# Optimization experiments

Hardware: AMD Instinct MI355X
Metric: run time of the kernel (lower is better)

The kernel has to match this reference:

```python
import jax, jax.numpy as jnp
import numpy as np


def _direction(x, W_in, conv_w, conv_b, W_xproj, A_log, D, W_out):
    # x: [b, l, d_model]
    b, L, _ = x.shape
    d_inner = A_log.shape[0]
    xz = x @ W_in.T                         # [b, l, 2*d_inner]
    xc, z = jnp.split(xz, 2, axis=-1)
    # depthwise causal conv1d (left pad d_conv-1, keep first L outputs)
    xt = jnp.transpose(xc, (0, 2, 1))       # [b, d_inner, l]
    k = conv_w.shape[-1]
    xt = jax.lax.conv_general_dilated(
        xt, conv_w, window_strides=(1,), padding=[(k - 1, 0)],
        dimension_numbers=("NCH", "OIH", "NCH"), feature_group_count=d_inner)
    xt = xt + conv_b[None, :, None]
    xc = jax.nn.silu(jnp.transpose(xt, (0, 2, 1)))  # [b, l, d_inner]
    proj = xc @ W_xproj.T                   # [b, l, d_inner + 2*n]
    n = (proj.shape[-1] - d_inner) // 2
    delta = jax.nn.softplus(proj[..., :d_inner])
    Bm = proj[..., d_inner:d_inner + n]
    Cm = proj[..., d_inner + n:]
    A = -jnp.exp(A_log)                     # [d_inner]

    def step(s, inp):
        u_t, dt, B_t, C_t = inp             # [b,d], [b,d], [b,n], [b,n]
        dA = jnp.exp(dt[..., None] * A[None, :, None])          # [b,d,n]
        s = dA * s + dt[..., None] * B_t[:, None, :] * u_t[..., None]
        y = jnp.einsum('bn,bdn->bd', C_t, s) + D * u_t
        return s, y

    s0 = jnp.zeros((b, d_inner, n), x.dtype)
    xs = (jnp.swapaxes(xc, 0, 1), jnp.swapaxes(delta, 0, 1),
          jnp.swapaxes(Bm, 0, 1), jnp.swapaxes(Cm, 0, 1))
    _, ys = jax.lax.scan(step, s0, xs)      # ys: [l, b, d_inner]
    y = jnp.swapaxes(ys, 0, 1)
    y = y * jax.nn.silu(z)
    return y @ W_out.T                      # [b, l, d_model]


def setup_inputs() -> dict:
    key = jax.random.key(0)
    ks = jax.random.split(key, 8)
    b, L, d_model, d_inner, n, k = 2, 1024, 512, 1024, 64, 4
    s = lambda kk, shape, sc=0.02: jax.random.normal(kk, shape, jnp.float32) * sc
    return {
        "x": jax.random.normal(ks[0], (b, L, d_model), jnp.float32),
        "W_in": s(ks[1], (2 * d_inner, d_model)),
        "conv_w": s(ks[2], (d_inner, 1, k), 0.1),
        "conv_b": s(ks[3], (d_inner,), 0.1),
        "W_xproj": s(ks[4], (d_inner + 2 * n, d_inner)),
        "A_log": jax.random.normal(ks[5], (d_inner,), jnp.float32),
        "D": jnp.ones((d_inner,), jnp.float32),
        "W_out": s(ks[6], (d_model, d_inner)),
    }


def reference(x, W_in, conv_w, conv_b, W_xproj, A_log, D, W_out):
    out_fwd = _direction(x, W_in, conv_w, conv_b, W_xproj, A_log, D, W_out)
    out_bwd = _direction(jnp.flip(x, axis=1), W_in, conv_w, conv_b, W_xproj, A_log, D, W_out)
    return 0.5 * (out_fwd + jnp.flip(out_bwd, axis=1))
```

## Files before the change

### kernel.cpp

```cpp
#include <hip/hip_runtime.h>
#include <math.h>

#define B_    2
#define LSEQ  1024
#define DM    512
#define DI    1024
#define NS    64
#define TC    32
#define NC    (LSEQ/TC)
#define LDP   72

typedef __bf16 bf16x8 __attribute__((ext_vector_type(8)));
typedef float  f32x4  __attribute__((ext_vector_type(4)));

__device__ __forceinline__ float fexp(float x)   { return __expf(x); }
__device__ __forceinline__ float sp_f(float x)   { return fmaxf(x, 0.f) + __logf(1.f + __expf(-fabsf(x))); }
__device__ __forceinline__ float silu_f(float x) { return x * __builtin_amdgcn_rcpf(1.f + __expf(-x)); }
__device__ __forceinline__ unsigned short f2bf(float f) {
    unsigned int u = __float_as_uint(f);
    u += 0x7FFF + ((u >> 16) & 1);
    return (unsigned short)(u >> 16);
}
__device__ __forceinline__ float bf2f(unsigned short h) {
    return __uint_as_float(((unsigned int)h) << 16);
}
__device__ __forceinline__ void gload16(const void* g, void* l) {
    __builtin_amdgcn_global_load_lds(
        (const __attribute__((address_space(1))) unsigned int*)g,
        (__attribute__((address_space(3))) unsigned int*)l, 16, 0, 0);
}

__global__ __launch_bounds__(256) void castall(
    const float* __restrict__ x, const float* __restrict__ W_in,
    const float* __restrict__ W_xproj, const float* __restrict__ W_out,
    unsigned short* __restrict__ xb, unsigned short* __restrict__ winb,
    unsigned short* __restrict__ wxb, unsigned short* __restrict__ wob)
{
    int i = (blockIdx.x * 256 + threadIdx.x) * 4;
    const float* s; unsigned short* dst; int off;
    if (i < 1048576)      { s = x;       dst = xb;   off = i; }
    else if (i < 2097152) { s = W_in;    dst = winb; off = i - 1048576; }
    else if (i < 3276800) { s = W_xproj; dst = wxb;  off = i - 2097152; }
    else                  { s = W_out;   dst = wob;  off = i - 3276800; }
    float4 v = *(const float4*)(s + off);
    ushort4 o;
    o.x = f2bf(v.x); o.y = f2bf(v.y); o.z = f2bf(v.z); o.w = f2bf(v.w);
    *(ushort4*)(dst + off) = o;
}

__global__ __launch_bounds__(256) void gemm64(
    const unsigned short* __restrict__ Alo, const unsigned short* __restrict__ Ahi,
    const unsigned short* __restrict__ B, float* __restrict__ C,
    int M, int N, int K, int wrapK, int ks, int mode,
    const float* __restrict__ A_log, const unsigned short* __restrict__ u_in,
    unsigned* __restrict__ ddu_out,
    unsigned short* __restrict__ Bbf, unsigned short* __restrict__ Cbf)
{
    __shared__ short As0[64 * 64];
    __shared__ short Bs0[64 * 64];
    __shared__ short As1[64 * 64];
    __shared__ short Bs1[64 * 64];
    const int tid  = threadIdx.x;
    const int lane = tid & 63, wid = tid >> 6;

    const int gx = gridDim.x;
    int id  = blockIdx.y * gx + blockIdx.x;
    int q   = (gx * gridDim.y) >> 3;
    int swz = (id & 7) * q + (id >> 3);
    const int bm = (swz / gx) * 64, bn = (swz % gx) * 64;

    const int wm = (wid >> 1) * 32, wn = (wid & 1) * 32;
    const int fr = lane & 15;
    const int h  = fr & 7;
    const int tq = lane >> 4;
    const int Kc = K / ks;
    const int k0beg = blockIdx.z * Kc;
    const int nsteps = Kc / 64;
    float* Cz = C + (size_t)blockIdx.z * M * N;
    unsigned short* Czb = (unsigned short*)C + (size_t)blockIdx.z * M * N;

    const unsigned short* Asrc;
    int ka0;
    if (k0beg >= wrapK) { Asrc = Ahi; ka0 = k0beg - wrapK; }
    else                { Asrc = Alo; ka0 = k0beg; }

    const char* pA[2];
    const char* pB[2];
#pragma unroll
    for (int r = 0; r < 2; r++) {
        int o    = tid * 16 + r * 4096;
        int row  = o >> 7;
        int colb = ((((o >> 4) & 7) ^ (row & 7)) << 4);
        pA[r] = (const char*)Asrc + ((size_t)(bm + row) * wrapK + ka0) * 2 + colb;
        pB[r] = (const char*)B    + ((size_t)(bn + row) * wrapK + ka0) * 2 + colb;
    }
    const int wbase = wid * 1024;

    f32x4 acc[2][2];
#pragma unroll
    for (int i = 0; i < 2; i++)
#pragma unroll
        for (int j = 0; j < 2; j++) acc[i][j] = (f32x4)0.f;

    auto STAGE = [&](short* Adst, short* Bdst) {
#pragma unroll
        for (int r = 0; r < 2; r++) { gload16(pA[r], (char*)Adst + wbase + r * 4096); pA[r] += 128; }
#pragma unroll
        for (int r = 0; r < 2; r++) { gload16(pB[r], (char*)Bdst + wbase + r * 4096); pB[r] += 128; }
    };
    auto COMPUTE = [&](const short* Asrc_l, const short* Bsrc_l) {
#pragma unroll
        for (int kk = 0; kk < 2; kk++) {
            const int sc = ((kk * 4 + tq) ^ h) << 3;
            bf16x8 af[2], bfr[2];
#pragma unroll
            for (int i = 0; i < 2; i++)
                af[i] = *reinterpret_cast<const bf16x8*>(&Asrc_l[(wm + i * 16 + fr) * 64 + sc]);
#pragma unroll
            for (int j = 0; j < 2; j++)
                bfr[j] = *reinterpret_cast<const bf16x8*>(&Bsrc_l[(wn + j * 16 + fr) * 64 + sc]);
#pragma unroll
            for (int i = 0; i < 2; i++)
#pragma unroll
                for (int j = 0; j < 2; j++)
                    acc[i][j] = __builtin_amdgcn_mfma_f32_16x16x32_bf16(af[i], bfr[j], acc[i][j], 0, 0, 0);
        }
    };

    STAGE(As0, Bs0);
    __syncthreads();
    for (int st = 0; st < nsteps; st += 2) {
        if (st + 1 < nsteps) STAGE(As1, Bs1);
        COMPUTE(As0, Bs0);
        __syncthreads();
        if (st + 1 < nsteps) {
            if (st + 2 < nsteps) STAGE(As0, Bs0);
            COMPUTE(As1, Bs1);
            __syncthreads();
        }
    }

    const int crow = (lane >> 4) * 4;
    if (mode == 2) {
        if (bn < 1024) {
#pragma unroll
            for (int j = 0; j < 2; j++) {
                int d = bn + wn + j * 16 + fr;
                float nAd = -fexp(A_log[d]);
#pragma unroll
                for (int i = 0; i < 2; i++)
#pragma unroll
                    for (int r = 0; r < 4; r++) {
                        int m = bm + wm + i * 16 + crow + r;
                        float delta = sp_f(acc[i][j][r]);
                        size_t idx = (size_t)m * DI + d;
                        float dA = fexp(delta * nAd);
                        float du = delta * bf2f(u_in[idx]);
                        ddu_out[idx] = (unsigned)f2bf(dA) | ((unsigned)f2bf(du) << 16);
                    }
            }
        } else {
#pragma unroll
            for (int j = 0; j < 2; j++) {
                int cc = bn + wn + j * 16 + fr;
#pragma unroll
                for (int i = 0; i < 2; i++)
#pragma unroll
                    for (int r = 0; r < 4; r++) {
                        int m = bm + wm + i * 16 + crow + r;
                        unsigned short v16 = f2bf(acc[i][j][r]);
                        if (cc < 1024 + NS) Bbf[(size_t)m * NS + cc - 1024]      = v16;
                        else                Cbf[(size_t)m * NS + cc - 1024 - NS] = v16;
                    }
            }
        }
    } else {
#pragma unroll
        for (int i = 0; i < 2; i++)
#pragma unroll
            for (int j = 0; j < 2; j++)
#pragma unroll
                for (int r = 0; r < 4; r++) {
                    size_t idx = (size_t)(bm + wm + i * 16 + crow + r) * N + (bn + wn + j * 16 + fr);
                    if (mode == 1) Czb[idx] = f2bf(acc[i][j][r]);
                    else           Cz[idx]  = acc[i][j][r];
                }
    }
}

__global__ __launch_bounds__(256) void reduce4(
    const float* __restrict__ p, float* __restrict__ out, int n)
{
    int i = (blockIdx.x * 256 + threadIdx.x) * 4;
    if (i >= n) return;
    float4 a = *(const float4*)(p + i);
    float4 b = *(const float4*)(p + n + i);
    float4 c = *(const float4*)(p + 2 * n + i);
    float4 d = *(const float4*)(p + 3 * n + i);
    float4 o;
    o.x = (a.x + b.x) + (c.x + d.x);
    o.y = (a.y + b.y) + (c.y + d.y);
    o.z = (a.z + b.z) + (c.z + d.z);
    o.w = (a.w + b.w) + (c.w + d.w);
    *(float4*)(out + i) = o;
}

__global__ __launch_bounds__(256) void convk(
    const unsigned short* __restrict__ xzb, const float* __restrict__ cw,
    const float* __restrict__ cb, const float* __restrict__ Dvec,
    unsigned short* __restrict__ uc2b, unsigned short* __restrict__ ygb,
    unsigned short* __restrict__ Fbuf)
{
    int idx = blockIdx.x * 256 + threadIdx.x;
    int b   = idx >> 18;
    int rem = idx & ((LSEQ * 256) - 1);
    int tau = rem >> 8;
    int d4  = (rem & 255) << 2;

    const unsigned short* xc = xzb + (size_t)b * LSEQ * (2 * DI);
    float xv[7][4];
#pragma unroll
    for (int rr = 0; rr < 7; rr++) {
        int t = tau - 3 + rr;
        if (t >= 0 && t < LSEQ) {
            ushort4 v = *(const ushort4*)&xc[(size_t)t * 2048 + d4];
            xv[rr][0] = bf2f(v.x); xv[rr][1] = bf2f(v.y);
            xv[rr][2] = bf2f(v.z); xv[rr][3] = bf2f(v.w);
        } else {
            xv[rr][0] = 0.f; xv[rr][1] = 0.f; xv[rr][2] = 0.f; xv[rr][3] = 0.f;
        }
    }
    ushort4 zv = *(const ushort4*)&xc[(size_t)tau * 2048 + DI + d4];
    float4 cbv = *(const float4*)&cb[d4];
    float4 Dv  = *(const float4*)&Dvec[d4];
    float cbA[4] = {cbv.x, cbv.y, cbv.z, cbv.w};
    float DA[4]  = {Dv.x, Dv.y, Dv.z, Dv.w};
    float zA[4]  = {bf2f(zv.x), bf2f(zv.y), bf2f(zv.z), bf2f(zv.w)};

    unsigned short ufb[4], ubb[4], yfb[4], ybb[4], Ff[4];
#pragma unroll
    for (int j = 0; j < 4; j++) {
        float4 w = *(const float4*)&cw[(size_t)(d4 + j) * 4];
        float accf = fmaf(w.x, xv[0][j], fmaf(w.y, xv[1][j], fmaf(w.z, xv[2][j], fmaf(w.w, xv[3][j], cbA[j]))));
        float accb = fmaf(w.x, xv[6][j], fmaf(w.y, xv[5][j], fmaf(w.z, xv[4][j], fmaf(w.w, xv[3][j], cbA[j]))));
        float uf = silu_f(accf), ub = silu_f(accb);
        ufb[j] = f2bf(uf); ubb[j] = f2bf(ub);
        yfb[j] = f2bf(DA[j] * uf); ybb[j] = f2bf(DA[j] * ub);
        Ff[j]  = f2bf(0.5f * silu_f(zA[j]));
    }
    size_t fi = ((size_t)b * LSEQ + tau) * DI + d4;
    size_t bi = ((size_t)(2 + b) * LSEQ + tau) * DI + d4;
    *(ushort4*)&uc2b[fi] = *(ushort4*)ufb;
    *(ushort4*)&uc2b[bi] = *(ushort4*)ubb;
    *(ushort4*)&ygb[fi]  = *(ushort4*)yfb;
    *(ushort4*)&ygb[bi]  = *(ushort4*)ybb;
    *(ushort4*)&Fbuf[fi] = *(ushort4*)Ff;
}

__global__ __launch_bounds__(256) void passA(
    const unsigned* __restrict__ ddu,
    const unsigned short* __restrict__ Bbf, const unsigned short* __restrict__ Cbf,
    unsigned short* __restrict__ ygb, unsigned short* __restrict__ gbuf,
    unsigned short* __restrict__ sEnd, float* __restrict__ Pbuf)
{
    const int dl   = threadIdx.x >> 2;
    const int nq   = threadIdx.x & 3;
    const int d0   = blockIdx.x * 64;
    const int d    = d0 + dl;
    const int c    = blockIdx.y;
    const int dirb = blockIdx.z;
    const int dir  = dirb >> 1;

    __shared__ float Bsh[TC][NS];
    __shared__ float Csh[TC][NS];
    __shared__ unsigned short gshY[TC][64];
    __shared__ unsigned short gshG[TC][64];

    for (int i = threadIdx.x * 4; i < TC * NS; i += 1024) {
        int tl = i >> 6, n = i & 63;
        int tau = dir ? (LSEQ - 1 - (c * TC + tl)) : (c * TC + tl);
        ushort4 vb = *(const ushort4*)&Bbf[((size_t)dirb * LSEQ + tau) * NS + n];
        ushort4 vc = *(const ushort4*)&Cbf[((size_t)dirb * LSEQ + tau) * NS + n];
        Bsh[tl][n+0] = bf2f(vb.x); Bsh[tl][n+1] = bf2f(vb.y);
        Bsh[tl][n+2] = bf2f(vb.z); Bsh[tl][n+3] = bf2f(vb.w);
        Csh[tl][n+0] = bf2f(vc.x); Csh[tl][n+1] = bf2f(vc.y);
        Csh[tl][n+2] = bf2f(vc.z); Csh[tl][n+3] = bf2f(vc.w);
    }
    __syncthreads();

    float s[16];
#pragma unroll
    for (int i = 0; i < 16; i++) s[i] = 0.f;
    float g_run = 1.f;

    int tau0 = dir ? (LSEQ - 1 - c * TC) : (c * TC);
    long stp = (dir ? -1L : 1L) * (long)DI;
    const unsigned* pW = ddu + ((size_t)dirb * LSEQ + tau0) * DI + d;
    const unsigned short* pY = ygb + ((size_t)dirb * LSEQ + tau0) * DI + d;

    unsigned w = *pW;
    float Du = bf2f(*pY);
    for (int tl = 0; tl < TC; tl++) {
        unsigned w_c = w;
        float Du_c = Du;
        if (tl + 1 < TC) {
            pW += stp; pY += stp;
            w = *pW; Du = bf2f(*pY);
        }
        float dA_c = bf2f((unsigned short)(w_c & 0xffff));
        float du_c = bf2f((unsigned short)(w_c >> 16));
        g_run *= dA_c;
        float ydot = 0.f;
        const float4* brow = (const float4*)&Bsh[tl][nq * 16];
        const float4* crow = (const float4*)&Csh[tl][nq * 16];
#pragma unroll
        for (int q = 0; q < 4; q++) {
            float4 bv = brow[q];
            float4 cv = crow[q];
            float s0 = fmaf(du_c, bv.x, dA_c * s[4*q+0]); s[4*q+0] = s0; ydot = fmaf(cv.x, s0, ydot);
            float s1 = fmaf(du_c, bv.y, dA_c * s[4*q+1]); s[4*q+1] = s1; ydot = fmaf(cv.y, s1, ydot);
            float s2 = fmaf(du_c, bv.z, dA_c * s[4*q+2]); s[4*q+2] = s2; ydot = fmaf(cv.z, s2, ydot);
            float s3 = fmaf(du_c, bv.w, dA_c * s[4*q+3]); s[4*q+3] = s3; ydot = fmaf(cv.w, s3, ydot);
        }
        ydot += __shfl_xor(ydot, 1);
        ydot += __shfl_xor(ydot, 2);
        if (nq == 0) {
            gshY[tl][dl] = f2bf(Du_c + ydot);
            gshG[tl][dl] = f2bf(g_run);
        }
    }
    __syncthreads();

    size_t base = (((size_t)dirb * NC + c) * DI + d) * NS + nq * 16;
#pragma unroll
    for (int q = 0; q < 4; q++) {
        ushort4 v;
        v.x = f2bf(s[4*q+0]); v.y = f2bf(s[4*q+1]);
        v.z = f2bf(s[4*q+2]); v.w = f2bf(s[4*q+3]);
        *(ushort4*)&sEnd[base + q * 4] = v;
    }
    if (nq == 0) Pbuf[((size_t)dirb * NC + c) * DI + d] = g_run;

    for (int i = threadIdx.x * 4; i < TC * 64; i += 1024) {
        int tl = i >> 6, col = i & 63;
        int tau = dir ? (LSEQ - 1 - (c * TC + tl)) : (c * TC + tl);
        *(ushort4*)&ygb[((size_t)dirb * LSEQ + tau) * DI + d0 + col]  = *(const ushort4*)&gshY[tl][col];
        *(ushort4*)&gbuf[((size_t)dirb * LSEQ + tau) * DI + d0 + col] = *(const ushort4*)&gshG[tl][col];
    }
}

__global__ __launch_bounds__(256) void passB(
    const unsigned* __restrict__ sEnd2, const float* __restrict__ Pbuf,
    unsigned* __restrict__ sInit2)
{
    const int fl   = blockIdx.x * 256 + threadIdx.x;
    const int dirb = blockIdx.y;
    const int d    = fl >> 5;
    float r0 = 0.f, r1 = 0.f;
    for (int c = 0; c < NC; c++) {
        size_t idx = ((size_t)(dirb * NC + c)) * (DI * NS / 2) + fl;
        unsigned v = sEnd2[idx];
        float t0 = bf2f((unsigned short)(v & 0xffff));
        float t1 = bf2f((unsigned short)(v >> 16));
        sInit2[idx] = (unsigned)f2bf(r0) | ((unsigned)f2bf(r1) << 16);
        float P = Pbuf[((size_t)dirb * NC + c) * DI + d];
        r0 = fmaf(P, r0, t0);
        r1 = fmaf(P, r1, t1);
    }
}

__global__ __launch_bounds__(256) void corrK(
    const unsigned short* __restrict__ Cbf, const unsigned short* __restrict__ sInitB,
    const unsigned short* __restrict__ gbuf, const unsigned short* __restrict__ Fbuf,
    unsigned short* __restrict__ ygb)
{
    const int tid  = threadIdx.x;
    const int lane = tid & 63, wid = tid >> 6;
    const int d0   = blockIdx.x * 128;
    const int c    = blockIdx.y;
    const int dirb = blockIdx.z;
    const int dir  = dirb >> 1;
    const int b    = dirb & 1;
    const int fr = lane & 15, fk = (lane >> 4) * 8;
    const int wn = wid * 32;

    __shared__ short Cs[TC * LDP];
    __shared__ short Ss[128 * LDP];
    __shared__ float corrS[TC * 128];

    for (int i = tid * 4; i < TC * 64; i += 1024) {
        int tl = i >> 6, n = i & 63;
        int tau = dir ? (LSEQ - 1 - (c * TC + tl)) : (c * TC + tl);
        *(ushort4*)&Cs[tl * LDP + n] = *(const ushort4*)&Cbf[((size_t)dirb * LSEQ + tau) * NS + n];
    }
    for (int i = tid * 4; i < 128 * 64; i += 1024) {
        int r = i >> 6, n = i & 63;
        *(ushort4*)&Ss[r * LDP + n] =
            *(const ushort4*)&sInitB[(((size_t)dirb * NC + c) * DI + d0 + r) * NS + n];
    }
    __syncthreads();

    f32x4 acc[2][2];
#pragma unroll
    for (int i = 0; i < 2; i++)
#pragma unroll
        for (int j = 0; j < 2; j++) acc[i][j] = (f32x4)0.f;

#pragma unroll
    for (int kk = 0; kk < 2; kk++) {
        bf16x8 af[2], bfr[2];
#pragma unroll
        for (int i = 0; i < 2; i++)
            af[i] = *reinterpret_cast<const bf16x8*>(&Cs[(i * 16 + fr) * LDP + kk * 32 + fk]);
#pragma unroll
        for (int j = 0; j < 2; j++)
            bfr[j] = *reinterpret_cast<const bf16x8*>(&Ss[(wn + j * 16 + fr) * LDP + kk * 32 + fk]);
#pragma unroll
        for (int i = 0; i < 2; i++)
#pragma unroll
            for (int j = 0; j < 2; j++)
                acc[i][j] = __builtin_amdgcn_mfma_f32_16x16x32_bf16(af[i], bfr[j], acc[i][j], 0, 0, 0);
    }

    const int crow = (lane >> 4) * 4;
#pragma unroll
    for (int i = 0; i < 2; i++)
#pragma unroll
        for (int j = 0; j < 2; j++)
#pragma unroll
            for (int r = 0; r < 4; r++)
                corrS[(i * 16 + crow + r) * 128 + (wn + j * 16 + fr)] = acc[i][j][r];
    __syncthreads();

    for (int i = tid * 4; i < TC * 128; i += 1024) {
        int tl = i >> 7, col = i & 127;
        int tau = dir ? (LSEQ - 1 - (c * TC + tl)) : (c * TC + tl);
        size_t gi = ((size_t)dirb * LSEQ + tau) * DI + d0 + col;
        size_t fi = ((size_t)b    * LSEQ + tau) * DI + d0 + col;
        ushort4 g4 = *(const ushort4*)&gbuf[gi];
        ushort4 y4 = *(const ushort4*)&ygb[gi];
        ushort4 F4 = *(const ushort4*)&Fbuf[fi];
        const float* cr = &corrS[tl * 128 + col];
        ushort4 o;
        o.x = f2bf(bf2f(F4.x) * fmaf(bf2f(g4.x), cr[0], bf2f(y4.x)));
        o.y = f2bf(bf2f(F4.y) * fmaf(bf2f(g4.y), cr[1], bf2f(y4.y)));
        o.z = f2bf(bf2f(F4.z) * fmaf(bf2f(g4.z), cr[2], bf2f(y4.z)));
        o.w = f2bf(bf2f(F4.w) * fmaf(bf2f(g4.w), cr[3], bf2f(y4.w)));
        *(ushort4*)&ygb[gi] = o;
    }
}

extern "C" void kernel_launch(void* const* d_in, const int* in_sizes, int n_in,
                              void* d_out, int out_size, void* d_ws, size_t ws_size,
                              hipStream_t stream)
{
    const float* x      = (const float*)d_in[0];
    const float* W_in   = (const float*)d_in[1];
    const float* conv_w = (const float*)d_in[2];
    const float* conv_b = (const float*)d_in[3];
    const float* W_xprj = (const float*)d_in[4];
    const float* A_log  = (const float*)d_in[5];
    const float* Dvec   = (const float*)d_in[6];
    const float* W_out  = (const float*)d_in[7];
    float* out = (float*)d_out;

    float* ws = (float*)d_ws;
    unsigned*       ddu   = (unsigned*)ws;
    unsigned short* uc2b  = (unsigned short*)(ws + 4194304);
    unsigned short* xzb   = uc2b + 4194304;
    unsigned short* ygb   = xzb  + 4194304;
    unsigned short* gbuf  = ygb  + 4194304;
    unsigned short* Fbuf  = gbuf + 4194304;
    unsigned short* Bbf   = Fbuf + 2097152;
    unsigned short* Cbf   = Bbf  + 262144;
    unsigned short* wob   = Cbf  + 262144;
    float*          Pbuf  = (float*)(wob + 524288);
    unsigned short* xb     = (unsigned short*)ddu;
    unsigned short* winb   = xb + 1048576;
    unsigned short* wxb    = gbuf;
    unsigned short* sEnd   = uc2b;
    unsigned short* sInitB = (unsigned short*)ddu;
    float*          gpart  = (float*)ddu;

    castall<<<3712, 256, 0, stream>>>(x, W_in, W_xprj, W_out, xb, winb, wxb, wob);

    gemm64<<<dim3(32, 32), 256, 0, stream>>>(xb, nullptr, winb, (float*)xzb,
        B_ * LSEQ, 2 * DI, DM, DM, 1, 1, nullptr, nullptr, nullptr, nullptr, nullptr);

    convk<<<2048, 256, 0, stream>>>(xzb, conv_w, conv_b, Dvec, uc2b, ygb, Fbuf);

    gemm64<<<dim3(18, 64), 256, 0, stream>>>(uc2b, nullptr, wxb, nullptr,
        4 * LSEQ, DI + 2 * NS, DI, DI, 1, 2, A_log, uc2b, ddu, Bbf, Cbf);

    passA<<<dim3(16, NC, 4), 256, 0, stream>>>(ddu, Bbf, Cbf, ygb, gbuf, sEnd, Pbuf);

    passB<<<dim3(128, 4), 256, 0, stream>>>((const unsigned*)sEnd, Pbuf, (unsigned*)sInitB);

    corrK<<<dim3(8, NC, 4), 256, 0, stream>>>(Cbf, sInitB, gbuf, Fbuf, ygb);

    gemm64<<<dim3(8, 32, 4), 256, 0, stream>>>(ygb, ygb + (size_t)2 * LSEQ * DI, wob, gpart,
        B_ * LSEQ, DM, 2 * DI, DI, 4, 0, nullptr, nullptr, nullptr, nullptr, nullptr);
    reduce4<<<1024, 256, 0, stream>>>(gpart, out, B_ * LSEQ * DM);
}
```

Baseline: 122.7 us.

## Replace LDS-staged GEMM with direct register-loaded MFMA operands

The GEMM kernel no longer stages A and B tiles through LDS with global_load_lds and double-buffered shared memory. Each wave now loads its MFMA fragments straight from global memory into registers, prefetching one K-step ahead, and drops all barriers. This removes LDS traffic and __syncthreads overhead. In exchange there is no data reuse across waves, so each operand is fetched by two waves and global and L2 traffic goes up. The per-lane 16-byte loads along rows are also less coalesced.

```diff
diff --git a/kernel.cpp b/kernel.cpp
--- a/kernel.cpp
+++ b/kernel.cpp
@@ -23,11 +23,6 @@
 }
 __device__ __forceinline__ float bf2f(unsigned short h) {
     return __uint_as_float(((unsigned int)h) << 16);
-}
-__device__ __forceinline__ void gload16(const void* g, void* l) {
-    __builtin_amdgcn_global_load_lds(
-        (const __attribute__((address_space(1))) unsigned int*)g,
-        (__attribute__((address_space(3))) unsigned int*)l, 16, 0, 0);
 }
 
 __global__ __launch_bounds__(256) void castall(
@@ -48,7 +43,7 @@
     *(ushort4*)(dst + off) = o;
 }
 
-__global__ __launch_bounds__(256) void gemm64(
+__global__ __launch_bounds__(256) void gemmreg(
     const unsigned short* __restrict__ Alo, const unsigned short* __restrict__ Ahi,
     const unsigned short* __restrict__ B, float* __restrict__ C,
     int M, int N, int K, int wrapK, int ks, int mode,
@@ -56,10 +51,6 @@
     unsigned* __restrict__ ddu_out,
     unsigned short* __restrict__ Bbf, unsigned short* __restrict__ Cbf)
 {
-    __shared__ short As0[64 * 64];
-    __shared__ short Bs0[64 * 64];
-    __shared__ short As1[64 * 64];
-    __shared__ short Bs1[64 * 64];
     const int tid  = threadIdx.x;
     const int lane = tid & 63, wid = tid >> 6;
 
@@ -70,12 +61,10 @@
     const int bm = (swz / gx) * 64, bn = (swz % gx) * 64;
 
     const int wm = (wid >> 1) * 32, wn = (wid & 1) * 32;
-    const int fr = lane & 15;
-    const int h  = fr & 7;
-    const int tq = lane >> 4;
+    const int fr = lane & 15, tq = lane >> 4;
     const int Kc = K / ks;
     const int k0beg = blockIdx.z * Kc;
-    const int nsteps = Kc / 64;
+    const int nsteps = Kc / 32;
     float* Cz = C + (size_t)blockIdx.z * M * N;
     unsigned short* Czb = (unsigned short*)C + (size_t)blockIdx.z * M * N;
 
@@ -84,17 +73,10 @@
     if (k0beg >= wrapK) { Asrc = Ahi; ka0 = k0beg - wrapK; }
     else                { Asrc = Alo; ka0 = k0beg; }
 
-    const char* pA[2];
-    const char* pB[2];
-#pragma unroll
-    for (int r = 0; r < 2; r++) {
-        int o    = tid * 16 + r * 4096;
-        int row  = o >> 7;
-        int colb = ((((o >> 4) & 7) ^ (row & 7)) << 4);
-        pA[r] = (const char*)Asrc + ((size_t)(bm + row) * wrapK + ka0) * 2 + colb;
-        pB[r] = (const char*)B    + ((size_t)(bn + row) * wrapK + ka0) * 2 + colb;
-    }
-    const int wbase = wid * 1024;
+    const char* pa0 = (const char*)(Asrc + (size_t)(bm + wm + fr) * wrapK + ka0 + tq * 8);
+    const char* pa1 = pa0 + (size_t)16 * wrapK * 2;
+    const char* pb0 = (const char*)(B + (size_t)(bn + wn + fr) * wrapK + ka0 + tq * 8);
+    const char* pb1 = pb0 + (size_t)16 * wrapK * 2;
 
     f32x4 acc[2][2];
 #pragma unroll
@@ -102,45 +84,28 @@
 #pragma unroll
         for (int j = 0; j < 2; j++) acc[i][j] = (f32x4)0.f;
 
-    auto STAGE = [&](short* Adst, short* Bdst) {
-#pragma unroll
-        for (int r = 0; r < 2; r++) { gload16(pA[r], (char*)Adst + wbase + r * 4096); pA[r] += 128; }
-#pragma unroll
-        for (int r = 0; r < 2; r++) { gload16(pB[r], (char*)Bdst + wbase + r * 4096); pB[r] += 128; }
-    };
-    auto COMPUTE = [&](const short* Asrc_l, const short* Bsrc_l) {
-#pragma unroll
-        for (int kk = 0; kk < 2; kk++) {
-            const int sc = ((kk * 4 + tq) ^ h) << 3;
-            bf16x8 af[2], bfr[2];
-#pragma unroll
-            for (int i = 0; i < 2; i++)
-                af[i] = *reinterpret_cast<const bf16x8*>(&Asrc_l[(wm + i * 16 + fr) * 64 + sc]);
-#pragma unroll
-            for (int j = 0; j < 2; j++)
-                bfr[j] = *reinterpret_cast<const bf16x8*>(&Bsrc_l[(wn + j * 16 + fr) * 64 + sc]);
-#pragma unroll
-            for (int i = 0; i < 2; i++)
-#pragma unroll
-                for (int j = 0; j < 2; j++)
-                    acc[i][j] = __builtin_amdgcn_mfma_f32_16x16x32_bf16(af[i], bfr[j], acc[i][j], 0, 0, 0);
-        }
-    };
-
-    STAGE(As0, Bs0);
-    __syncthreads();
-    for (int st = 0; st < nsteps; st += 2) {
-        if (st + 1 < nsteps) STAGE(As1, Bs1);
-        COMPUTE(As0, Bs0);
-        __syncthreads();
+    bf16x8 a0 = *(const bf16x8*)pa0;
+    bf16x8 a1 = *(const bf16x8*)pa1;
+    bf16x8 b0 = *(const bf16x8*)pb0;
+    bf16x8 b1 = *(const bf16x8*)pb1;
+
+    for (int st = 0; st < nsteps; ++st) {
+        bf16x8 na0, na1, nb0, nb1;
         if (st + 1 < nsteps) {
-            if (st + 2 < nsteps) STAGE(As0, Bs0);
-            COMPUTE(As1, Bs1);
-            __syncthreads();
-        }
-    }
-
-    const int crow = (lane >> 4) * 4;
+            pa0 += 64; pa1 += 64; pb0 += 64; pb1 += 64;
+            na0 = *(const bf16x8*)pa0;
+            na1 = *(const bf16x8*)pa1;
+            nb0 = *(const bf16x8*)pb0;
+            nb1 = *(const bf16x8*)pb1;
+        }
+        acc[0][0] = __builtin_amdgcn_mfma_f32_16x16x32_bf16(a0, b0, acc[0][0], 0, 0, 0);
+        acc[0][1] = __builtin_amdgcn_mfma_f32_16x16x32_bf16(a0, b1, acc[0][1], 0, 0, 0);
+        acc[1][0] = __builtin_amdgcn_mfma_f32_16x16x32_bf16(a1, b0, acc[1][0], 0, 0, 0);
+        acc[1][1] = __builtin_amdgcn_mfma_f32_16x16x32_bf16(a1, b1, acc[1][1], 0, 0, 0);
+        a0 = na0; a1 = na1; b0 = nb0; b1 = nb1;
+    }
+
+    const int crow = tq * 4;
     if (mode == 2) {
         if (bn < 1024) {
 #pragma unroll
@@ -484,12 +449,12 @@
 
     castall<<<3712, 256, 0, stream>>>(x, W_in, W_xprj, W_out, xb, winb, wxb, wob);
 
-    gemm64<<<dim3(32, 32), 256, 0, stream>>>(xb, nullptr, winb, (float*)xzb,
+    gemmreg<<<dim3(32, 32), 256, 0, stream>>>(xb, nullptr, winb, (float*)xzb,
         B_ * LSEQ, 2 * DI, DM, DM, 1, 1, nullptr, nullptr, nullptr, nullptr, nullptr);
 
     convk<<<2048, 256, 0, stream>>>(xzb, conv_w, conv_b, Dvec, uc2b, ygb, Fbuf);
 
-    gemm64<<<dim3(18, 64), 256, 0, stream>>>(uc2b, nullptr, wxb, nullptr,
+    gemmreg<<<dim3(18, 64), 256, 0, stream>>>(uc2b, nullptr, wxb, nullptr,
         4 * LSEQ, DI + 2 * NS, DI, DI, 1, 2, A_log, uc2b, ddu, Bbf, Cbf);
 
     passA<<<dim3(16, NC, 4), 256, 0, stream>>>(ddu, Bbf, Cbf, ygb, gbuf, sEnd, Pbuf);
@@ -498,7 +463,7 @@
 
     corrK<<<dim3(8, NC, 4), 256, 0, stream>>>(Cbf, sInitB, gbuf, Fbuf, ygb);
 
-    gemm64<<<dim3(8, 32, 4), 256, 0, stream>>>(ygb, ygb + (size_t)2 * LSEQ * DI, wob, gpart,
+    gemmreg<<<dim3(8, 32, 4), 256, 0, stream>>>(ygb, ygb + (size_t)2 * LSEQ * DI, wob, gpart,
         B_ * LSEQ, DM, 2 * DI, DI, 4, 0, nullptr, nullptr, nullptr, nullptr, nullptr);
     reduce4<<<1024, 256, 0, stream>>>(gpart, out, B_ * LSEQ * DM);
 }
```

Result: slower. 215.3 us (+75.6%).
